# Performance work log

Hardware: AMD Instinct MI355X
Metric: run time of the kernel (lower is better)

The kernel has to match this reference:

```python
import jax, jax.numpy as jnp
import numpy as np

D_MODEL = 1024
NUM_HEADS = 16
D_KEY = D_MODEL // NUM_HEADS


def setup_inputs() -> dict:
    key = jax.random.key(0)
    ks = jax.random.split(key, 9)
    B, S = 2, 2048
    s = 1.0 / np.sqrt(D_MODEL)
    return {
        "x": jax.random.normal(ks[0], (B, S, D_MODEL), dtype=jnp.float32),
        "W_q": jax.random.normal(ks[1], (D_MODEL, D_MODEL), dtype=jnp.float32) * s,
        "b_q": jnp.zeros((D_MODEL,), dtype=jnp.float32),
        "W_k": jax.random.normal(ks[2], (D_MODEL, D_MODEL), dtype=jnp.float32) * s,
        "b_k": jnp.zeros((D_MODEL,), dtype=jnp.float32),
        "W_v": jax.random.normal(ks[3], (D_MODEL, D_MODEL), dtype=jnp.float32) * s,
        "b_v": jnp.zeros((D_MODEL,), dtype=jnp.float32),
        "W_o": jax.random.normal(ks[4], (D_MODEL, D_MODEL), dtype=jnp.float32) * s,
        "b_o": jnp.zeros((D_MODEL,), dtype=jnp.float32),
    }


def reference(x, W_q, b_q, W_k, b_k, W_v, b_v, W_o, b_o):
    B, S, _ = x.shape
    # Linear projections (torch nn.Linear: x @ W.T + b; here W stored as [in, out])
    Q = x @ W_q + b_q
    K = x @ W_k + b_k
    V = x @ W_v + b_v
    # [B, S, H, dk] -> [B, H, S, dk]
    def split_heads(t):
        return t.reshape(B, S, NUM_HEADS, D_KEY).transpose(0, 2, 1, 3)
    Q, K, V = split_heads(Q), split_heads(K), split_heads(V)
    scale = 1.0 / np.sqrt(D_KEY).astype(np.float32)
    logits = jnp.einsum("bhqd,bhkd->bhqk", Q, K) * scale  # [B,H,S,S]
    weights = jax.nn.softmax(logits, axis=-1)
    ctx = jnp.einsum("bhqk,bhkd->bhqd", weights, V)       # [B,H,S,dk]
    concat = ctx.transpose(0, 2, 1, 3).reshape(B, S, D_MODEL)
    return concat @ W_o + b_o
```

## Files before the change

kernel.cpp:

```cpp
#include <hip/hip_runtime.h>
#include <cstdint>
#include <cstddef>

#define SEQ   2048
#define NH    16
#define DK    64
#define DM    1024
#define MTOT  4096
#define QSCALE (0.125f * 1.44269504088896f)

typedef __attribute__((ext_vector_type(8))) short           short8;
typedef __attribute__((ext_vector_type(8))) unsigned short  ushort8;
typedef __attribute__((ext_vector_type(4))) unsigned short  ushort4v;
typedef __attribute__((ext_vector_type(2))) unsigned int    uint2v;
typedef __attribute__((ext_vector_type(4))) float           float4v;
typedef unsigned short u16;
typedef unsigned int   u32;

__device__ inline float4v mfma16(short8 a, short8 b, float4v c) {
    return __builtin_amdgcn_mfma_f32_16x16x32_bf16(a, b, c, 0, 0, 0);
}
__device__ inline u16 f2bf(float f) {
    u32 u = __float_as_uint(f);
    u += 0x7fffu + ((u >> 16) & 1u);
    return (u16)(u >> 16);
}
__device__ inline u32 pkbf(float a, float b) {
    u32 ua = __float_as_uint(a) + 0x8000u;
    u32 ub = __float_as_uint(b) + 0x8000u;
    return __builtin_amdgcn_perm(ub, ua, 0x07060302);
}
__device__ inline void gld16(const void* g, void* lds) {
    __builtin_amdgcn_global_load_lds(
        (const __attribute__((address_space(1))) u32*)g,
        (__attribute__((address_space(3))) u32*)lds, 16, 0, 0);
}

__global__ __launch_bounds__(256)
void convert_x(const float* __restrict__ x, u16* __restrict__ xb)
{
    const int i = blockIdx.x * 256 + threadIdx.x;
    const float4v a = ((const float4v*)x)[2 * i];
    const float4v b = ((const float4v*)x)[2 * i + 1];
    ushort8 o;
    #pragma unroll
    for (int j = 0; j < 4; j++) { o[j] = f2bf(a[j]); o[4 + j] = f2bf(b[j]); }
    ((ushort8*)xb)[i] = o;
}

__global__ __launch_bounds__(256)
void transpose_w(const float* __restrict__ W0, const float* __restrict__ W1,
                 const float* __restrict__ W2, const float* __restrict__ W3,
                 u16* __restrict__ T0, u16* __restrict__ T1,
                 u16* __restrict__ T2, u16* __restrict__ T3)
{
    __shared__ u16 t[64][68];
    const float* W; u16* T;
    switch (blockIdx.z) {
        case 0: W = W0; T = T0; break;
        case 1: W = W1; T = T1; break;
        case 2: W = W2; T = T2; break;
        default: W = W3; T = T3; break;
    }
    const int n0 = blockIdx.x * 64, k0 = blockIdx.y * 64;
    const int r  = threadIdx.x >> 4;
    const int c4 = (threadIdx.x & 15) * 4;
    #pragma unroll
    for (int i = 0; i < 4; i++) {
        float4v v = *(const float4v*)&W[(size_t)(k0 + r + i * 16) * DM + n0 + c4];
        #pragma unroll
        for (int j = 0; j < 4; j++) t[r + i * 16][c4 + j] = f2bf(v[j]);
    }
    __syncthreads();
    #pragma unroll
    for (int i = 0; i < 4; i++) {
        const int rr = r + i * 16;
        ushort4v o;
        #pragma unroll
        for (int j = 0; j < 4; j++) o[j] = t[c4 + j][rr];
        *(ushort4v*)&T[(size_t)(n0 + rr) * DM + k0 + c4] = o;
    }
}

__global__ __launch_bounds__(256)
void transpose_v(const u16* __restrict__ V, u16* __restrict__ VT)
{
    __shared__ u16 t[64][80];
    const int kv0 = blockIdx.x * 64;
    const size_t head = (size_t)blockIdx.y * SEQ * DK;
    const int r = threadIdx.x >> 3;
    const int c = (threadIdx.x & 7) * 8;
    #pragma unroll
    for (int i = 0; i < 2; i++) {
        const int row = r + i * 32;
        ushort8 v = *(const ushort8*)&V[head + (size_t)(kv0 + row) * DK + c];
        #pragma unroll
        for (int j = 0; j < 8; j++) t[c + j][row] = v[j];
    }
    __syncthreads();
    #pragma unroll
    for (int i = 0; i < 2; i++) {
        const int d = (threadIdx.x >> 3) + i * 32;
        *(ushort8*)&VT[head + (size_t)d * SEQ + kv0 + c] = *(const ushort8*)&t[d][c];
    }
}

template<int TM, int MODE>
__global__ __launch_bounds__(TM * 4)
void gemm_bt(const u16* __restrict__ A, const u16* __restrict__ WT,
             const float* __restrict__ bq, const float* __restrict__ bk,
             const float* __restrict__ bv,
             void* __restrict__ out0, u16* __restrict__ outK, u16* __restrict__ outV)
{
    constexpr int NT = TM * 4;
    __shared__ u16 Al[TM][64];
    __shared__ u16 Bl[128][64];
    const int tid  = threadIdx.x;
    const int lane = tid & 63, w = tid >> 6;
    const int quad = lane >> 4, l16 = lane & 15;
    const int n0 = blockIdx.x * 128, m0 = blockIdx.y * TM;
    const int wm = (TM == 128) ? (w >> 2) * 64 : 0;
    const int wn = (TM == 128) ? (w & 3) * 32 : w * 32;

    float4v acc[4][2] = {};

    for (int k0 = 0; k0 < DM; k0 += 64) {
        __syncthreads();
        #pragma unroll
        for (int j = 0; j < TM * 8 / NT; j++) {
            const int c = j * NT + tid;
            const int row = c >> 3, kc = c & 7;
            gld16(A + (size_t)(m0 + row) * DM + k0 + ((kc ^ (row & 7)) * 8),
                  &Al[0][0] + (size_t)(j * NT + w * 64) * 8);
        }
        #pragma unroll
        for (int j = 0; j < 1024 / NT; j++) {
            const int c = j * NT + tid;
            const int row = c >> 3, kc = c & 7;
            gld16(WT + (size_t)(n0 + row) * DM + k0 + ((kc ^ (row & 7)) * 8),
                  &Bl[0][0] + (size_t)(j * NT + w * 64) * 8);
        }
        __syncthreads();
        #pragma unroll
        for (int u = 0; u < 2; u++) {
            short8 af[4], bf[2];
            #pragma unroll
            for (int mi = 0; mi < 4; mi++) {
                const int row = wm + mi * 16 + l16;
                af[mi] = *(const short8*)&Al[row][((4 * u + quad) ^ (row & 7)) * 8];
            }
            #pragma unroll
            for (int ni = 0; ni < 2; ni++) {
                const int row = wn + ni * 16 + l16;
                bf[ni] = *(const short8*)&Bl[row][((4 * u + quad) ^ (row & 7)) * 8];
            }
            #pragma unroll
            for (int mi = 0; mi < 4; mi++)
                #pragma unroll
                for (int ni = 0; ni < 2; ni++)
                    acc[mi][ni] = mfma16(af[mi], bf[ni], acc[mi][ni]);
        }
    }

    if constexpr (MODE == 0) {
        float* out = (float*)out0;
        #pragma unroll
        for (int ni = 0; ni < 2; ni++) {
            const int col = n0 + wn + ni * 16 + l16;
            const float bb = bq[col];
            #pragma unroll
            for (int mi = 0; mi < 4; mi++)
                #pragma unroll
                for (int r = 0; r < 4; r++) {
                    const int row = m0 + wm + mi * 16 + quad * 4 + r;
                    out[(size_t)row * DM + col] = acc[mi][ni][r] + bb;
                }
        }
    } else {
        const int seg = n0 >> 10;
        u16* outp = (seg == 0) ? (u16*)out0 : (seg == 1 ? outK : outV);
        const float* bias = (seg == 0) ? bq : (seg == 1 ? bk : bv);
        const float scl = (seg == 0) ? QSCALE : 1.0f;
        #pragma unroll
        for (int ni = 0; ni < 2; ni++) {
            const int col = (n0 & 1023) + wn + ni * 16 + l16;
            const float bb = bias[col];
            const int h = col >> 6, d = col & 63;
            #pragma unroll
            for (int mi = 0; mi < 4; mi++)
                #pragma unroll
                for (int r = 0; r < 4; r++) {
                    const int row = m0 + wm + mi * 16 + quad * 4 + r;
                    const int b = row >> 11, s = row & (SEQ - 1);
                    outp[(((size_t)(b * NH + h) * SEQ + s) << 6) + d] =
                        f2bf((acc[mi][ni][r] + bb) * scl);
                }
        }
    }
}

__global__ __launch_bounds__(256)
void attn_kernel(const u16* __restrict__ Q, const u16* __restrict__ K,
                 const u16* __restrict__ VT, u16* __restrict__ Ctx)
{
    __shared__ u16 Kl[2][64][64];
    __shared__ u16 Vl[2][64][64];
    __shared__ u16 Pl[4][2][16][88];

    const int tid  = threadIdx.x;
    const int lane = tid & 63, w = tid >> 6;
    const int quad = lane >> 4, l16 = lane & 15;
    const int qt = blockIdx.x;
    const int bh = blockIdx.y;
    const size_t head = (size_t)bh * SEQ * DK;

    short8 qf[2][2];
    #pragma unroll
    for (int g = 0; g < 2; g++) {
        const size_t qrow = head + (size_t)(qt * 128 + w * 32 + g * 16 + l16) * DK;
        qf[g][0] = *(const short8*)(Q + qrow + quad * 8);
        qf[g][1] = *(const short8*)(Q + qrow + 32 + quad * 8);
    }

    float4v acc[2][4] = {};
    float l_part[2] = {0.f, 0.f};

    auto stage = [&](int kv0, int buf) {
        #pragma unroll
        for (int j = 0; j < 2; j++) {
            const int c = j * 256 + tid;
            const int row = c >> 3, kc = c & 7;
            gld16(K + head + (size_t)(kv0 + row) * DK + ((kc ^ (row & 7)) * 8),
                  &Kl[buf][0][0] + (size_t)(j * 256 + w * 64) * 8);
            gld16(VT + head + (size_t)row * SEQ + kv0 + ((kc ^ (row & 7)) * 8),
                  &Vl[buf][0][0] + (size_t)(j * 256 + w * 64) * 8);
        }
    };

    stage(0, 0);
    for (int it = 0; it < SEQ / 64; it++) {
        const int cur = it & 1;
        __syncthreads();
        if (it + 1 < SEQ / 64) stage((it + 1) * 64, cur ^ 1);

        #pragma unroll
        for (int t = 0; t < 4; t++) {
            const int row = t * 16 + l16;
            const short8 kf0 = *(const short8*)&Kl[cur][row][(quad ^ (row & 7)) * 8];
            const short8 kf1 = *(const short8*)&Kl[cur][row][((4 + quad) ^ (row & 7)) * 8];
            #pragma unroll
            for (int g = 0; g < 2; g++) {
                float4v z = {};
                z = mfma16(kf0, qf[g][0], z);
                z = mfma16(kf1, qf[g][1], z);
                float p0 = exp2f(z[0]), p1 = exp2f(z[1]);
                float p2 = exp2f(z[2]), p3 = exp2f(z[3]);
                l_part[g] += (p0 + p1) + (p2 + p3);
                uint2v pk; pk[0] = pkbf(p0, p1); pk[1] = pkbf(p2, p3);
                *(uint2v*)&Pl[w][g][l16][t * 16 + quad * 4] = pk;
            }
        }

        short8 pf[2][2];
        #pragma unroll
        for (int g = 0; g < 2; g++) {
            pf[g][0] = *(const short8*)&Pl[w][g][l16][quad * 8];
            pf[g][1] = *(const short8*)&Pl[w][g][l16][32 + quad * 8];
        }
        #pragma unroll
        for (int t = 0; t < 4; t++) {
            const int row = t * 16 + l16;
            const short8 vf0 = *(const short8*)&Vl[cur][row][(quad ^ (row & 7)) * 8];
            const short8 vf1 = *(const short8*)&Vl[cur][row][((4 + quad) ^ (row & 7)) * 8];
            #pragma unroll
            for (int g = 0; g < 2; g++) {
                acc[g][t] = mfma16(vf0, pf[g][0], acc[g][t]);
                acc[g][t] = mfma16(vf1, pf[g][1], acc[g][t]);
            }
        }
    }

    const int b = bh >> 4, h = bh & 15;
    #pragma unroll
    for (int g = 0; g < 2; g++) {
        float l = l_part[g];
        l += __shfl_xor(l, 16);
        l += __shfl_xor(l, 32);
        const float rl = 1.0f / l;
        #pragma unroll
        for (int t = 0; t < 4; t++) {
            uint2v ok;
            ok[0] = pkbf(acc[g][t][0] * rl, acc[g][t][1] * rl);
            ok[1] = pkbf(acc[g][t][2] * rl, acc[g][t][3] * rl);
            *(uint2v*)&Pl[w][g][l16][t * 16 + quad * 4] = ok;
        }
    }
    const int rowq = lane >> 2, ch = lane & 3;
    #pragma unroll
    for (int g = 0; g < 2; g++) {
        const int s = qt * 128 + w * 32 + g * 16 + rowq;
        ushort8 o0 = *(const ushort8*)&Pl[w][g][rowq][ch * 16];
        ushort8 o1 = *(const ushort8*)&Pl[w][g][rowq][ch * 16 + 8];
        u16* dst = Ctx + (size_t)(b * SEQ + s) * DM + h * 64 + ch * 16;
        *(ushort8*)dst = o0;
        *(ushort8*)(dst + 8) = o1;
    }
}

extern "C" void kernel_launch(void* const* d_in, const int* in_sizes, int n_in,
                              void* d_out, int out_size, void* d_ws, size_t ws_size,
                              hipStream_t stream)
{
    const float* x   = (const float*)d_in[0];
    const float* W_q = (const float*)d_in[1];
    const float* b_q = (const float*)d_in[2];
    const float* W_k = (const float*)d_in[3];
    const float* b_k = (const float*)d_in[4];
    const float* W_v = (const float*)d_in[5];
    const float* b_v = (const float*)d_in[6];
    const float* W_o = (const float*)d_in[7];
    const float* b_o = (const float*)d_in[8];

    u16* xb  = (u16*)d_ws;
    u16* WT  = xb + (size_t)MTOT * DM;
    u16* WTo = WT + (size_t)3 * DM * DM;
    u16* Vb  = WTo + (size_t)DM * DM;
    u16* VTb = Vb + (size_t)MTOT * DM;
    u16* Cb  = xb;
    u16* Qb  = (u16*)d_out;
    u16* Kb  = Qb + (size_t)MTOT * DM;

    convert_x<<<2048, 256, 0, stream>>>(x, xb);
    transpose_w<<<dim3(16, 16, 4), 256, 0, stream>>>(
        W_q, W_k, W_v, W_o, WT, WT + (size_t)DM * DM, WT + (size_t)2 * DM * DM, WTo);
    gemm_bt<128, 1><<<dim3(24, 32), 512, 0, stream>>>(xb, WT, b_q, b_k, b_v, Qb, Kb, Vb);
    transpose_v<<<dim3(SEQ / 64, 2 * NH), 256, 0, stream>>>(Vb, VTb);
    attn_kernel<<<dim3(SEQ / 128, 2 * NH), 256, 0, stream>>>(Qb, Kb, VTb, Cb);
    gemm_bt<64, 0><<<dim3(8, 64), 256, 0, stream>>>(Cb, WTo, b_o, nullptr, nullptr,
                                                    (float*)d_out, nullptr, nullptr);
}
```

Before: 213.9 us.

## Shrink attention tiles to 64 queries and 32-key blocks for higher occupancy

The attention kernel now gives each block 64 query rows (one 16-row group per wave) and walks K/V in 32-key blocks, which halves LDS per block and requests 4 blocks per CU through launch bounds. The grid doubles to 1024 blocks and V uses a new XOR swizzle for its 32-wide rows. Explicit lgkmcnt waits are added before the P and output readback from LDS. In exchange, each wave reuses every K/V fragment half as often, and the loop runs twice as many iterations with the same number of barriers per iteration, so sync and global-to-LDS traffic per FLOP go up.

```diff
diff --git a/kernel.cpp b/kernel.cpp
--- a/kernel.cpp
+++ b/kernel.cpp
@@ -35,6 +35,7 @@
         (const __attribute__((address_space(1))) u32*)g,
         (__attribute__((address_space(3))) u32*)lds, 16, 0, 0);
 }
+#define LGKM_FENCE() asm volatile("s_waitcnt lgkmcnt(0)" ::: "memory")
 
 __global__ __launch_bounds__(256)
 void convert_x(const float* __restrict__ x, u16* __restrict__ xb)
@@ -199,13 +200,14 @@
     }
 }
 
-__global__ __launch_bounds__(256)
+__global__ __launch_bounds__(256, 4)
 void attn_kernel(const u16* __restrict__ Q, const u16* __restrict__ K,
                  const u16* __restrict__ VT, u16* __restrict__ Ctx)
 {
-    __shared__ u16 Kl[2][64][64];
-    __shared__ u16 Vl[2][64][64];
-    __shared__ u16 Pl[4][2][16][88];
+    __shared__ u16 Kl[2][32][64];
+    __shared__ u16 Vl[2][64][32];
+    __shared__ u16 Pl[4][16][40];
+    __shared__ u16 Ol[4][16][72];
 
     const int tid  = threadIdx.x;
     const int lane = tid & 63, w = tid >> 6;
@@ -214,97 +216,76 @@
     const int bh = blockIdx.y;
     const size_t head = (size_t)bh * SEQ * DK;
 
-    short8 qf[2][2];
-    #pragma unroll
-    for (int g = 0; g < 2; g++) {
-        const size_t qrow = head + (size_t)(qt * 128 + w * 32 + g * 16 + l16) * DK;
-        qf[g][0] = *(const short8*)(Q + qrow + quad * 8);
-        qf[g][1] = *(const short8*)(Q + qrow + 32 + quad * 8);
-    }
-
-    float4v acc[2][4] = {};
-    float l_part[2] = {0.f, 0.f};
-
-    auto stage = [&](int kv0, int buf) {
-        #pragma unroll
-        for (int j = 0; j < 2; j++) {
-            const int c = j * 256 + tid;
-            const int row = c >> 3, kc = c & 7;
-            gld16(K + head + (size_t)(kv0 + row) * DK + ((kc ^ (row & 7)) * 8),
-                  &Kl[buf][0][0] + (size_t)(j * 256 + w * 64) * 8);
-            gld16(VT + head + (size_t)row * SEQ + kv0 + ((kc ^ (row & 7)) * 8),
-                  &Vl[buf][0][0] + (size_t)(j * 256 + w * 64) * 8);
-        }
-    };
-
-    stage(0, 0);
-    for (int it = 0; it < SEQ / 64; it++) {
+    const size_t qrow = head + (size_t)(qt * 64 + w * 16 + l16) * DK;
+    const short8 qf0 = *(const short8*)(Q + qrow + quad * 8);
+    const short8 qf1 = *(const short8*)(Q + qrow + 32 + quad * 8);
+
+    float4v acc[4] = {};
+    float l_part = 0.f;
+
+    const int rK = tid >> 3, cK = tid & 7;
+    const int rV = tid >> 2, cV = tid & 3;
+    const int sV = (rV & 3) ^ ((rV >> 2) & 3);
+    const u16* const Kg = K  + head + (size_t)rK * DK  + (cK ^ (rK & 7)) * 8;
+    const u16* const Vg = VT + head + (size_t)rV * SEQ + (cV ^ sV) * 8;
+
+    gld16(Kg, &Kl[0][0][0] + tid * 8);
+    gld16(Vg, &Vl[0][0][0] + tid * 8);
+
+    for (int it = 0; it < SEQ / 32; it++) {
         const int cur = it & 1;
         __syncthreads();
-        if (it + 1 < SEQ / 64) stage((it + 1) * 64, cur ^ 1);
-
-        #pragma unroll
-        for (int t = 0; t < 4; t++) {
+        if (it + 1 < SEQ / 32) {
+            gld16(Kg + (size_t)(it + 1) * 32 * DK, &Kl[cur ^ 1][0][0] + tid * 8);
+            gld16(Vg + (size_t)(it + 1) * 32,      &Vl[cur ^ 1][0][0] + tid * 8);
+        }
+
+        #pragma unroll
+        for (int t = 0; t < 2; t++) {
             const int row = t * 16 + l16;
             const short8 kf0 = *(const short8*)&Kl[cur][row][(quad ^ (row & 7)) * 8];
             const short8 kf1 = *(const short8*)&Kl[cur][row][((4 + quad) ^ (row & 7)) * 8];
-            #pragma unroll
-            for (int g = 0; g < 2; g++) {
-                float4v z = {};
-                z = mfma16(kf0, qf[g][0], z);
-                z = mfma16(kf1, qf[g][1], z);
-                float p0 = exp2f(z[0]), p1 = exp2f(z[1]);
-                float p2 = exp2f(z[2]), p3 = exp2f(z[3]);
-                l_part[g] += (p0 + p1) + (p2 + p3);
-                uint2v pk; pk[0] = pkbf(p0, p1); pk[1] = pkbf(p2, p3);
-                *(uint2v*)&Pl[w][g][l16][t * 16 + quad * 4] = pk;
-            }
-        }
-
-        short8 pf[2][2];
-        #pragma unroll
-        for (int g = 0; g < 2; g++) {
-            pf[g][0] = *(const short8*)&Pl[w][g][l16][quad * 8];
-            pf[g][1] = *(const short8*)&Pl[w][g][l16][32 + quad * 8];
-        }
+            float4v z = {};
+            z = mfma16(kf0, qf0, z);
+            z = mfma16(kf1, qf1, z);
+            const float p0 = exp2f(z[0]), p1 = exp2f(z[1]);
+            const float p2 = exp2f(z[2]), p3 = exp2f(z[3]);
+            l_part += (p0 + p1) + (p2 + p3);
+            uint2v pk; pk[0] = pkbf(p0, p1); pk[1] = pkbf(p2, p3);
+            *(uint2v*)&Pl[w][l16][t * 16 + quad * 4] = pk;
+        }
+        LGKM_FENCE();
+        const short8 pf = *(const short8*)&Pl[w][l16][quad * 8];
+
         #pragma unroll
         for (int t = 0; t < 4; t++) {
-            const int row = t * 16 + l16;
-            const short8 vf0 = *(const short8*)&Vl[cur][row][(quad ^ (row & 7)) * 8];
-            const short8 vf1 = *(const short8*)&Vl[cur][row][((4 + quad) ^ (row & 7)) * 8];
-            #pragma unroll
-            for (int g = 0; g < 2; g++) {
-                acc[g][t] = mfma16(vf0, pf[g][0], acc[g][t]);
-                acc[g][t] = mfma16(vf1, pf[g][1], acc[g][t]);
-            }
-        }
-    }
-
+            const int d = t * 16 + l16;
+            const short8 vf =
+                *(const short8*)&Vl[cur][d][(quad ^ ((d & 3) ^ ((d >> 2) & 3))) * 8];
+            acc[t] = mfma16(vf, pf, acc[t]);
+        }
+    }
+
+    float l = l_part;
+    l += __shfl_xor(l, 16);
+    l += __shfl_xor(l, 32);
+    const float rl = 1.0f / l;
+    #pragma unroll
+    for (int t = 0; t < 4; t++) {
+        uint2v ok;
+        ok[0] = pkbf(acc[t][0] * rl, acc[t][1] * rl);
+        ok[1] = pkbf(acc[t][2] * rl, acc[t][3] * rl);
+        *(uint2v*)&Ol[w][l16][t * 16 + quad * 4] = ok;
+    }
+    LGKM_FENCE();
     const int b = bh >> 4, h = bh & 15;
-    #pragma unroll
-    for (int g = 0; g < 2; g++) {
-        float l = l_part[g];
-        l += __shfl_xor(l, 16);
-        l += __shfl_xor(l, 32);
-        const float rl = 1.0f / l;
-        #pragma unroll
-        for (int t = 0; t < 4; t++) {
-            uint2v ok;
-            ok[0] = pkbf(acc[g][t][0] * rl, acc[g][t][1] * rl);
-            ok[1] = pkbf(acc[g][t][2] * rl, acc[g][t][3] * rl);
-            *(uint2v*)&Pl[w][g][l16][t * 16 + quad * 4] = ok;
-        }
-    }
     const int rowq = lane >> 2, ch = lane & 3;
-    #pragma unroll
-    for (int g = 0; g < 2; g++) {
-        const int s = qt * 128 + w * 32 + g * 16 + rowq;
-        ushort8 o0 = *(const ushort8*)&Pl[w][g][rowq][ch * 16];
-        ushort8 o1 = *(const ushort8*)&Pl[w][g][rowq][ch * 16 + 8];
-        u16* dst = Ctx + (size_t)(b * SEQ + s) * DM + h * 64 + ch * 16;
-        *(ushort8*)dst = o0;
-        *(ushort8*)(dst + 8) = o1;
-    }
+    const int s = qt * 64 + w * 16 + rowq;
+    const ushort8 o0 = *(const ushort8*)&Ol[w][rowq][ch * 16];
+    const ushort8 o1 = *(const ushort8*)&Ol[w][rowq][ch * 16 + 8];
+    u16* dst = Ctx + (size_t)(b * SEQ + s) * DM + h * 64 + ch * 16;
+    *(ushort8*)dst = o0;
+    *(ushort8*)(dst + 8) = o1;
 }
 
 extern "C" void kernel_launch(void* const* d_in, const int* in_sizes, int n_in,
@@ -335,7 +316,7 @@
         W_q, W_k, W_v, W_o, WT, WT + (size_t)DM * DM, WT + (size_t)2 * DM * DM, WTo);
     gemm_bt<128, 1><<<dim3(24, 32), 512, 0, stream>>>(xb, WT, b_q, b_k, b_v, Qb, Kb, Vb);
     transpose_v<<<dim3(SEQ / 64, 2 * NH), 256, 0, stream>>>(Vb, VTb);
-    attn_kernel<<<dim3(SEQ / 128, 2 * NH), 256, 0, stream>>>(Qb, Kb, VTb, Cb);
+    attn_kernel<<<dim3(SEQ / 64, 2 * NH), 256, 0, stream>>>(Qb, Kb, VTb, Cb);
     gemm_bt<64, 0><<<dim3(8, 64), 256, 0, stream>>>(Cb, WTo, b_o, nullptr, nullptr,
                                                     (float*)d_out, nullptr, nullptr);
 }
```

After: 207.7 us. -2.9%, faster.

## Split attention KV range across two wave groups and fuse V transpose into GEMM

Applied to the files above, without the earlier changes.

The QKV GEMM epilogue now writes V directly in transposed [d][s] layout with packed stores, which removes the separate transpose_v kernel and its extra round trip through memory. The attention kernel goes to 512 threads, and two wave groups each process half of the KV sequence in 32-row tiles with a new LDS swizzle. Their partial accumulators and row sums are reduced through shared memory at the end, and output stores are simplified. This raises parallelism per block and removes one launch, at the cost of an LDS reduction, extra barriers and more LDS use per block.

```diff
diff --git a/kernel.cpp b/kernel.cpp
--- a/kernel.cpp
+++ b/kernel.cpp
@@ -35,6 +35,7 @@
         (const __attribute__((address_space(1))) u32*)g,
         (__attribute__((address_space(3))) u32*)lds, 16, 0, 0);
 }
+#define LGKM_FENCE() asm volatile("s_waitcnt lgkmcnt(0)" ::: "memory")
 
 __global__ __launch_bounds__(256)
 void convert_x(const float* __restrict__ x, u16* __restrict__ xb)
@@ -79,29 +80,6 @@
         #pragma unroll
         for (int j = 0; j < 4; j++) o[j] = t[c4 + j][rr];
         *(ushort4v*)&T[(size_t)(n0 + rr) * DM + k0 + c4] = o;
-    }
-}
-
-__global__ __launch_bounds__(256)
-void transpose_v(const u16* __restrict__ V, u16* __restrict__ VT)
-{
-    __shared__ u16 t[64][80];
-    const int kv0 = blockIdx.x * 64;
-    const size_t head = (size_t)blockIdx.y * SEQ * DK;
-    const int r = threadIdx.x >> 3;
-    const int c = (threadIdx.x & 7) * 8;
-    #pragma unroll
-    for (int i = 0; i < 2; i++) {
-        const int row = r + i * 32;
-        ushort8 v = *(const ushort8*)&V[head + (size_t)(kv0 + row) * DK + c];
-        #pragma unroll
-        for (int j = 0; j < 8; j++) t[c + j][row] = v[j];
-    }
-    __syncthreads();
-    #pragma unroll
-    for (int i = 0; i < 2; i++) {
-        const int d = (threadIdx.x >> 3) + i * 32;
-        *(ushort8*)&VT[head + (size_t)d * SEQ + kv0 + c] = *(const ushort8*)&t[d][c];
     }
 }
 
@@ -181,34 +159,54 @@
         u16* outp = (seg == 0) ? (u16*)out0 : (seg == 1 ? outK : outV);
         const float* bias = (seg == 0) ? bq : (seg == 1 ? bk : bv);
         const float scl = (seg == 0) ? QSCALE : 1.0f;
-        #pragma unroll
-        for (int ni = 0; ni < 2; ni++) {
-            const int col = (n0 & 1023) + wn + ni * 16 + l16;
-            const float bb = bias[col];
-            const int h = col >> 6, d = col & 63;
-            #pragma unroll
-            for (int mi = 0; mi < 4; mi++)
-                #pragma unroll
-                for (int r = 0; r < 4; r++) {
-                    const int row = m0 + wm + mi * 16 + quad * 4 + r;
-                    const int b = row >> 11, s = row & (SEQ - 1);
-                    outp[(((size_t)(b * NH + h) * SEQ + s) << 6) + d] =
-                        f2bf((acc[mi][ni][r] + bb) * scl);
+        if (seg < 2) {
+            #pragma unroll
+            for (int ni = 0; ni < 2; ni++) {
+                const int col = (n0 & 1023) + wn + ni * 16 + l16;
+                const float bb = bias[col];
+                const int h = col >> 6, d = col & 63;
+                #pragma unroll
+                for (int mi = 0; mi < 4; mi++)
+                    #pragma unroll
+                    for (int r = 0; r < 4; r++) {
+                        const int row = m0 + wm + mi * 16 + quad * 4 + r;
+                        const int b = row >> 11, s = row & (SEQ - 1);
+                        outp[(((size_t)(b * NH + h) * SEQ + s) << 6) + d] =
+                            f2bf((acc[mi][ni][r] + bb) * scl);
+                    }
+            }
+        } else {
+            #pragma unroll
+            for (int ni = 0; ni < 2; ni++) {
+                const int col = (n0 & 1023) + wn + ni * 16 + l16;
+                const float bb = bias[col];
+                const int h = col >> 6, d = col & 63;
+                #pragma unroll
+                for (int mi = 0; mi < 4; mi++) {
+                    const int row0 = m0 + wm + mi * 16 + quad * 4;
+                    const int b = row0 >> 11, s = row0 & (SEQ - 1);
+                    uint2v pv;
+                    pv[0] = pkbf(acc[mi][ni][0] + bb, acc[mi][ni][1] + bb);
+                    pv[1] = pkbf(acc[mi][ni][2] + bb, acc[mi][ni][3] + bb);
+                    *(uint2v*)&outp[(((size_t)((b * NH + h) * DK + d)) << 11) + s] = pv;
                 }
-        }
-    }
-}
-
-__global__ __launch_bounds__(256)
+            }
+        }
+    }
+}
+
+__global__ __launch_bounds__(512, 4)
 void attn_kernel(const u16* __restrict__ Q, const u16* __restrict__ K,
                  const u16* __restrict__ VT, u16* __restrict__ Ctx)
 {
-    __shared__ u16 Kl[2][64][64];
-    __shared__ u16 Vl[2][64][64];
-    __shared__ u16 Pl[4][2][16][88];
+    __shared__ u16 Kl[2][2][32][64];
+    __shared__ u16 Vl[2][2][64][32];
+    __shared__ u16 Pl[8][32][40];
+    __shared__ float Xl[4][64][17];
 
     const int tid  = threadIdx.x;
     const int lane = tid & 63, w = tid >> 6;
+    const int wq = w & 3, wgrp = w >> 2;
     const int quad = lane >> 4, l16 = lane & 15;
     const int qt = blockIdx.x;
     const int bh = blockIdx.y;
@@ -217,7 +215,7 @@
     short8 qf[2][2];
     #pragma unroll
     for (int g = 0; g < 2; g++) {
-        const size_t qrow = head + (size_t)(qt * 128 + w * 32 + g * 16 + l16) * DK;
+        const size_t qrow = head + (size_t)(qt * 128 + wq * 32 + g * 16 + l16) * DK;
         qf[g][0] = *(const short8*)(Q + qrow + quad * 8);
         qf[g][1] = *(const short8*)(Q + qrow + 32 + quad * 8);
     }
@@ -225,85 +223,106 @@
     float4v acc[2][4] = {};
     float l_part[2] = {0.f, 0.f};
 
-    auto stage = [&](int kv0, int buf) {
-        #pragma unroll
-        for (int j = 0; j < 2; j++) {
-            const int c = j * 256 + tid;
-            const int row = c >> 3, kc = c & 7;
-            gld16(K + head + (size_t)(kv0 + row) * DK + ((kc ^ (row & 7)) * 8),
-                  &Kl[buf][0][0] + (size_t)(j * 256 + w * 64) * 8);
-            gld16(VT + head + (size_t)row * SEQ + kv0 + ((kc ^ (row & 7)) * 8),
-                  &Vl[buf][0][0] + (size_t)(j * 256 + w * 64) * 8);
-        }
-    };
-
-    stage(0, 0);
-    for (int it = 0; it < SEQ / 64; it++) {
+    const int sh = tid >> 8;
+    const int rK = (tid >> 3) & 31, cK = tid & 7;
+    const int dV = (tid >> 2) & 63, cV = tid & 3;
+    const int sVk = (dV & 3) ^ ((dV >> 2) & 3);
+    const u16* const Kg = K  + head + (size_t)(sh * 1024 + rK) * DK + (cK ^ (rK & 7)) * 8;
+    const u16* const Vg = VT + head + (size_t)dV * SEQ + sh * 1024 + (cV ^ sVk) * 8;
+    u16* const Kdst = &Kl[0][0][0][0] + tid * 8;
+    u16* const Vdst = &Vl[0][0][0][0] + tid * 8;
+
+    gld16(Kg, Kdst);
+    gld16(Vg, Vdst);
+
+    for (int it = 0; it < 32; it++) {
         const int cur = it & 1;
         __syncthreads();
-        if (it + 1 < SEQ / 64) stage((it + 1) * 64, cur ^ 1);
-
-        #pragma unroll
-        for (int t = 0; t < 4; t++) {
+        if (it + 1 < 32) {
+            gld16(Kg + (size_t)(it + 1) * 32 * DK, Kdst + (cur ^ 1) * 4096);
+            gld16(Vg + (size_t)(it + 1) * 32,      Vdst + (cur ^ 1) * 4096);
+        }
+
+        #pragma unroll
+        for (int t = 0; t < 2; t++) {
             const int row = t * 16 + l16;
-            const short8 kf0 = *(const short8*)&Kl[cur][row][(quad ^ (row & 7)) * 8];
-            const short8 kf1 = *(const short8*)&Kl[cur][row][((4 + quad) ^ (row & 7)) * 8];
+            const short8 kf0 = *(const short8*)&Kl[cur][wgrp][row][(quad ^ (row & 7)) * 8];
+            const short8 kf1 = *(const short8*)&Kl[cur][wgrp][row][((4 + quad) ^ (row & 7)) * 8];
             #pragma unroll
             for (int g = 0; g < 2; g++) {
                 float4v z = {};
                 z = mfma16(kf0, qf[g][0], z);
                 z = mfma16(kf1, qf[g][1], z);
-                float p0 = exp2f(z[0]), p1 = exp2f(z[1]);
-                float p2 = exp2f(z[2]), p3 = exp2f(z[3]);
+                const float p0 = exp2f(z[0]), p1 = exp2f(z[1]);
+                const float p2 = exp2f(z[2]), p3 = exp2f(z[3]);
                 l_part[g] += (p0 + p1) + (p2 + p3);
                 uint2v pk; pk[0] = pkbf(p0, p1); pk[1] = pkbf(p2, p3);
-                *(uint2v*)&Pl[w][g][l16][t * 16 + quad * 4] = pk;
-            }
-        }
-
-        short8 pf[2][2];
+                *(uint2v*)&Pl[w][g * 16 + l16][t * 16 + quad * 4] = pk;
+            }
+        }
+        LGKM_FENCE();
+        short8 pf[2];
+        pf[0] = *(const short8*)&Pl[w][l16][quad * 8];
+        pf[1] = *(const short8*)&Pl[w][16 + l16][quad * 8];
+
+        #pragma unroll
+        for (int t = 0; t < 4; t++) {
+            const int d = t * 16 + l16;
+            const short8 vf =
+                *(const short8*)&Vl[cur][wgrp][d][(quad ^ ((d & 3) ^ ((d >> 2) & 3))) * 8];
+            acc[0][t] = mfma16(vf, pf[0], acc[0][t]);
+            acc[1][t] = mfma16(vf, pf[1], acc[1][t]);
+        }
+    }
+
+    #pragma unroll
+    for (int g = 0; g < 2; g++) {
+        l_part[g] += __shfl_xor(l_part[g], 16);
+        l_part[g] += __shfl_xor(l_part[g], 32);
+    }
+
+    float ltot[2];
+    #pragma unroll
+    for (int p = 0; p < 2; p++) {
+        __syncthreads();
+        if (wgrp == 1) {
+            #pragma unroll
+            for (int g = 0; g < 2; g++)
+                #pragma unroll
+                for (int tt = 0; tt < 2; tt++)
+                    #pragma unroll
+                    for (int r = 0; r < 4; r++)
+                        Xl[wq][lane][g * 8 + tt * 4 + r] = acc[g][2 * p + tt][r];
+            Xl[wq][lane][16] = l_part[p];
+        }
+        __syncthreads();
+        if (wgrp == 0) {
+            #pragma unroll
+            for (int g = 0; g < 2; g++)
+                #pragma unroll
+                for (int tt = 0; tt < 2; tt++)
+                    #pragma unroll
+                    for (int r = 0; r < 4; r++)
+                        acc[g][2 * p + tt][r] += Xl[wq][lane][g * 8 + tt * 4 + r];
+            ltot[p] = l_part[p] + Xl[wq][lane][16];
+        }
+    }
+
+    if (wgrp == 0) {
+        const int b = bh >> 4, h = bh & 15;
         #pragma unroll
         for (int g = 0; g < 2; g++) {
-            pf[g][0] = *(const short8*)&Pl[w][g][l16][quad * 8];
-            pf[g][1] = *(const short8*)&Pl[w][g][l16][32 + quad * 8];
-        }
-        #pragma unroll
-        for (int t = 0; t < 4; t++) {
-            const int row = t * 16 + l16;
-            const short8 vf0 = *(const short8*)&Vl[cur][row][(quad ^ (row & 7)) * 8];
-            const short8 vf1 = *(const short8*)&Vl[cur][row][((4 + quad) ^ (row & 7)) * 8];
-            #pragma unroll
-            for (int g = 0; g < 2; g++) {
-                acc[g][t] = mfma16(vf0, pf[g][0], acc[g][t]);
-                acc[g][t] = mfma16(vf1, pf[g][1], acc[g][t]);
-            }
-        }
-    }
-
-    const int b = bh >> 4, h = bh & 15;
-    #pragma unroll
-    for (int g = 0; g < 2; g++) {
-        float l = l_part[g];
-        l += __shfl_xor(l, 16);
-        l += __shfl_xor(l, 32);
-        const float rl = 1.0f / l;
-        #pragma unroll
-        for (int t = 0; t < 4; t++) {
-            uint2v ok;
-            ok[0] = pkbf(acc[g][t][0] * rl, acc[g][t][1] * rl);
-            ok[1] = pkbf(acc[g][t][2] * rl, acc[g][t][3] * rl);
-            *(uint2v*)&Pl[w][g][l16][t * 16 + quad * 4] = ok;
-        }
-    }
-    const int rowq = lane >> 2, ch = lane & 3;
-    #pragma unroll
-    for (int g = 0; g < 2; g++) {
-        const int s = qt * 128 + w * 32 + g * 16 + rowq;
-        ushort8 o0 = *(const ushort8*)&Pl[w][g][rowq][ch * 16];
-        ushort8 o1 = *(const ushort8*)&Pl[w][g][rowq][ch * 16 + 8];
-        u16* dst = Ctx + (size_t)(b * SEQ + s) * DM + h * 64 + ch * 16;
-        *(ushort8*)dst = o0;
-        *(ushort8*)(dst + 8) = o1;
+            const float rl = 1.0f / ltot[g];
+            const int s = qt * 128 + wq * 32 + g * 16 + l16;
+            u16* dst = Ctx + (size_t)(b * SEQ + s) * DM + h * 64 + quad * 4;
+            #pragma unroll
+            for (int t = 0; t < 4; t++) {
+                uint2v ov;
+                ov[0] = pkbf(acc[g][t][0] * rl, acc[g][t][1] * rl);
+                ov[1] = pkbf(acc[g][t][2] * rl, acc[g][t][3] * rl);
+                *(uint2v*)&dst[t * 16] = ov;
+            }
+        }
     }
 }
 
@@ -324,8 +343,7 @@
     u16* xb  = (u16*)d_ws;
     u16* WT  = xb + (size_t)MTOT * DM;
     u16* WTo = WT + (size_t)3 * DM * DM;
-    u16* Vb  = WTo + (size_t)DM * DM;
-    u16* VTb = Vb + (size_t)MTOT * DM;
+    u16* VTb = WTo + (size_t)DM * DM;
     u16* Cb  = xb;
     u16* Qb  = (u16*)d_out;
     u16* Kb  = Qb + (size_t)MTOT * DM;
@@ -333,9 +351,8 @@
     convert_x<<<2048, 256, 0, stream>>>(x, xb);
     transpose_w<<<dim3(16, 16, 4), 256, 0, stream>>>(
         W_q, W_k, W_v, W_o, WT, WT + (size_t)DM * DM, WT + (size_t)2 * DM * DM, WTo);
-    gemm_bt<128, 1><<<dim3(24, 32), 512, 0, stream>>>(xb, WT, b_q, b_k, b_v, Qb, Kb, Vb);
-    transpose_v<<<dim3(SEQ / 64, 2 * NH), 256, 0, stream>>>(Vb, VTb);
-    attn_kernel<<<dim3(SEQ / 128, 2 * NH), 256, 0, stream>>>(Qb, Kb, VTb, Cb);
+    gemm_bt<128, 1><<<dim3(24, 32), 512, 0, stream>>>(xb, WT, b_q, b_k, b_v, Qb, Kb, VTb);
+    attn_kernel<<<dim3(SEQ / 128, 2 * NH), 512, 0, stream>>>(Qb, Kb, VTb, Cb);
     gemm_bt<64, 0><<<dim3(8, 64), 256, 0, stream>>>(Cb, WTo, b_o, nullptr, nullptr,
                                                     (float*)d_out, nullptr, nullptr);
 }
```

Result: faster. 198.6 us (-7.1%).
